# Kernel tuning notes

Hardware: AMD Instinct MI355X
Metric: run time of the kernel (lower is better)

The kernel has to match this reference:

```python
import jax, jax.numpy as jnp
import numpy as np

E = 8       # expert_number
TOP_K = 2


def setup_inputs() -> dict:
    key = jax.random.key(0)
    ks = jax.random.split(key, 5)
    B, S, D, H = 4, 2048, 1024, 4096
    scale = 0.02
    return {
        "x": jax.random.normal(ks[0], (B, S, D), dtype=jnp.float32),
        "gate_w": jax.random.normal(ks[1], (D, E), dtype=jnp.float32) * scale,
        "gate_b": jnp.zeros((E,), dtype=jnp.float32),
        "w1": jax.random.normal(ks[2], (E, D, H), dtype=jnp.float32) * scale,
        "b1": jnp.zeros((E, H), dtype=jnp.float32),
        "w2": jax.random.normal(ks[3], (E, H, D), dtype=jnp.float32) * scale,
        "b2": jnp.zeros((E, D), dtype=jnp.float32),
    }


def reference(x, gate_w, gate_b, w1, b1, w2, b2):
    B, S, D = x.shape
    h = x.reshape(-1, D)                                   # [T, D]

    # Router: softmax in fp32, top-k, renormalize (matches torch code)
    router_logits = h @ gate_w + gate_b                    # [T, E]
    probs = jax.nn.softmax(router_logits.astype(jnp.float32), axis=-1)
    rw, sel = jax.lax.top_k(probs, TOP_K)                  # [T, K] each
    rw = rw / rw.sum(axis=-1, keepdims=True)
    rw = rw.astype(h.dtype)

    # Per-token combine weight for each expert (0 if not selected): [T, E]
    we = (jax.nn.one_hot(sel, E, dtype=h.dtype) * rw[..., None]).sum(axis=1)

    out = jnp.zeros_like(h)
    for e in range(E):  # fixed small expert count; per-expert GEMM + weighted combine
        mid = jax.nn.gelu(h @ w1[e] + b1[e], approximate=False)  # [T, H]
        ye = mid @ w2[e] + b2[e]                                 # [T, D]
        out = out + we[:, e:e + 1] * ye

    return out.reshape(B, S, D), router_logits
```

## Files before the change

kernel.cpp:

```cpp
#include <hip/hip_runtime.h>
#include <hip/hip_bf16.h>
#include <math.h>

#define T_TOKENS 8192
#define DDIM 1024
#define HDIM 4096
#define NEXP 8
#define CAP 8192
#define MAXTILES 136

typedef __bf16 bf16;
typedef __bf16 bf16x4 __attribute__((ext_vector_type(4)));
typedef __bf16 bf16x8 __attribute__((ext_vector_type(8)));
typedef float  floatx16 __attribute__((ext_vector_type(16)));

__device__ static inline void async_load16(const void* g, void* l)
{
    __builtin_amdgcn_global_load_lds(
        (const __attribute__((address_space(1))) void*)g,
        (__attribute__((address_space(3))) void*)l, 16, 0, 0);
}

__global__ void router_kernel(const float* __restrict__ x,
                              const float* __restrict__ gw,
                              const float* __restrict__ gbias,
                              float* __restrict__ logits_out,
                              int* counts, int* token_of, float* wtab,
                              int* selpack)
{
    int t = blockIdx.x * 4 + (threadIdx.x >> 6);
    int l = threadIdx.x & 63;
    const float4* xr = (const float4*)(x + (size_t)t * DDIM);

    float p[NEXP];
#pragma unroll
    for (int e = 0; e < NEXP; ++e) p[e] = 0.f;

#pragma unroll
    for (int it = 0; it < 4; ++it) {
        int d4 = it * 64 + l;
        float4 v = xr[d4];
        float vv[4] = {v.x, v.y, v.z, v.w};
#pragma unroll
        for (int j = 0; j < 4; ++j) {
            const float4* g4 = (const float4*)(gw + (size_t)(d4 * 4 + j) * NEXP);
            float4 ga = g4[0], gb4 = g4[1];
            p[0] += vv[j] * ga.x;  p[1] += vv[j] * ga.y;
            p[2] += vv[j] * ga.z;  p[3] += vv[j] * ga.w;
            p[4] += vv[j] * gb4.x; p[5] += vv[j] * gb4.y;
            p[6] += vv[j] * gb4.z; p[7] += vv[j] * gb4.w;
        }
    }
#pragma unroll
    for (int e = 0; e < NEXP; ++e) {
#pragma unroll
        for (int off = 32; off; off >>= 1) p[e] += __shfl_xor(p[e], off);
        p[e] += gbias[e];
    }
    if (l < NEXP) logits_out[(size_t)t * NEXP + l] = p[l];

    if (l == 0) {
        int e0 = 0;
#pragma unroll
        for (int e = 1; e < NEXP; ++e) if (p[e] > p[e0]) e0 = e;
        int e1 = -1;
#pragma unroll
        for (int e = 0; e < NEXP; ++e) {
            if (e == e0) continue;
            if (e1 < 0 || p[e] > p[e1]) e1 = e;
        }
        float w0 = 1.f / (1.f + expf(p[e1] - p[e0]));
        float w1 = 1.f / (1.f + expf(p[e0] - p[e1]));
        int s0 = atomicAdd(&counts[e0], 1);
        int s1 = atomicAdd(&counts[e1], 1);
        token_of[e0 * CAP + s0] = t;
        token_of[e1 * CAP + s1] = t;
        wtab[e0 * CAP + s0] = w0;
        wtab[e1 * CAP + s1] = w1;
        selpack[t] = e0 | (e1 << 8);
    }
}

__global__ void offsets_kernel(const int* __restrict__ counts,
                               int* __restrict__ offsets,
                               int* __restrict__ tiles)
{
    if (threadIdx.x == 0) {
        int tmp[MAXTILES];
        int a = 0, nt = 0;
        for (int e = 0; e < NEXP; ++e) {
            offsets[e] = a;
            for (int r = 0; r < counts[e]; r += 128)
                tmp[nt++] = (e << 24) | (a + r);
            a += counts[e];
        }
        offsets[NEXP] = a;
        int per = (nt + 7) >> 3;
        for (int p = 0; p < MAXTILES; ++p) {
            int c = p & 7, k = p >> 3;
            int src = c * per + k;
            tiles[p] = (k < per && src < nt) ? tmp[src] : -1;
        }
    }
}

__global__ void gather_kernel(const float* __restrict__ x,
                              const int* __restrict__ offsets,
                              const int* __restrict__ token_of,
                              bf16* __restrict__ xg)
{
    int row = blockIdx.x * 4 + (threadIdx.x >> 6);
    int l = threadIdx.x & 63;
    int e = 0;
#pragma unroll
    for (int i = 1; i < NEXP; ++i) e += (row >= offsets[i]);
    int t = token_of[e * CAP + (row - offsets[e])];
    const float4* src = (const float4*)(x + (size_t)t * DDIM);
    bf16x4* dst = (bf16x4*)(xg + (size_t)row * DDIM);
#pragma unroll
    for (int it = 0; it < 4; ++it) {
        float4 v = src[it * 64 + l];
        bf16x4 b;
        b[0] = (bf16)v.x; b[1] = (bf16)v.y; b[2] = (bf16)v.z; b[3] = (bf16)v.w;
        dst[it * 64 + l] = b;
    }
}

__global__ void transpose_cvt_kernel(const float* __restrict__ in,
                                     bf16* __restrict__ out, int R, int C)
{
    __shared__ bf16 tile[64][68];
    int e = blockIdx.z;
    const float* src = in + (size_t)e * R * C;
    bf16* dst = out + (size_t)e * R * C;
    int r0 = blockIdx.y * 64, c0 = blockIdx.x * 64;
    int t = threadIdx.x;
    int lr = t >> 4, c4 = t & 15;
#pragma unroll
    for (int it = 0; it < 4; ++it) {
        int r = lr + it * 16;
        float4 v = *(const float4*)(src + (size_t)(r0 + r) * C + c0 + c4 * 4);
        bf16x4 b;
        b[0] = (bf16)v.x; b[1] = (bf16)v.y; b[2] = (bf16)v.z; b[3] = (bf16)v.w;
        *(bf16x4*)(&tile[r][c4 * 4]) = b;
    }
    __syncthreads();
    int oc = t >> 3, rseg = (t & 7) * 8;
#pragma unroll
    for (int it = 0; it < 2; ++it) {
        int c = oc + it * 32;
        bf16x8 v;
#pragma unroll
        for (int j = 0; j < 8; ++j) v[j] = tile[rseg + j][c];
        *(bf16x8*)(dst + (size_t)(c0 + c) * R + r0 + rseg) = v;
    }
}

template<int KTOT>
__device__ static inline void stage_tile(const bf16* __restrict__ gbase,
                                         bf16* lds, int wave, int lane, int valid)
{
#pragma unroll
    for (int it = 0; it < 4; ++it) {
        int rbase = wave * 32 + it * 8;
        int rloc  = rbase + (lane >> 3);
        int grow  = rloc < valid ? rloc : (valid - 1);
        int chunk = (lane & 7) ^ (rloc & 7);
        const bf16* g = gbase + (size_t)grow * KTOT + chunk * 8;
        async_load16(g, lds + rbase * 64);
    }
}

__device__ static inline float fast_gelu(float v)
{
    float z = v * (2.302236479f + 0.1029451170f * v * v);
    float ex = __builtin_amdgcn_exp2f(z);
    return v * ex * __builtin_amdgcn_rcpf(ex + 1.f);
}

#define GEMM_CORE(KTOT)                                                        \
    int tid = threadIdx.x;                                                     \
    int lane = tid & 63, wave = tid >> 6;                                      \
    int wr = wave >> 1, wc = wave & 1;                                         \
    int m32 = lane & 31, khalf = lane >> 5;                                    \
    int swz = m32 & 7;                                                         \
    floatx16 acc[2][2];                                                        \
    _Pragma("unroll") for (int i = 0; i < 2; ++i)                              \
    _Pragma("unroll") for (int j = 0; j < 2; ++j)                              \
    _Pragma("unroll") for (int r = 0; r < 16; ++r) acc[i][j][r] = 0.f;         \
    for (int k0 = 0; k0 < KTOT; k0 += 64) {                                    \
        stage_tile<KTOT>(A + k0, As, wave, lane, valid);                       \
        stage_tile<KTOT>(B + k0, Bs, wave, lane, 128);                         \
        __syncthreads();                                                       \
        _Pragma("unroll") for (int s = 0; s < 4; ++s) {                        \
            int pofs = (((2 * s + khalf) ^ swz) * 8);                          \
            bf16x8 af[2], bfr[2];                                              \
            _Pragma("unroll") for (int i = 0; i < 2; ++i)                      \
                af[i] = *(const bf16x8*)(&As[(wr * 64 + i * 32 + m32) * 64 + pofs]); \
            _Pragma("unroll") for (int j = 0; j < 2; ++j)                      \
                bfr[j] = *(const bf16x8*)(&Bs[(wc * 64 + j * 32 + m32) * 64 + pofs]); \
            _Pragma("unroll") for (int i = 0; i < 2; ++i)                      \
            _Pragma("unroll") for (int j = 0; j < 2; ++j)                      \
                acc[i][j] = __builtin_amdgcn_mfma_f32_32x32x16_bf16(           \
                    af[i], bfr[j], acc[i][j], 0, 0, 0);                        \
        }                                                                      \
        __syncthreads();                                                       \
    }

__global__ __launch_bounds__(256, 4)
void moe_gemm1(const bf16* __restrict__ Abase, const bf16* __restrict__ Bbase,
               const float* __restrict__ bias, bf16* __restrict__ Out,
               const int* __restrict__ tiles, const int* __restrict__ offsets)
{
    int info = tiles[blockIdx.x];
    if (info < 0) return;
    int e = info >> 24, row0 = info & 0xffffff;
    int valid = offsets[e + 1] - row0; if (valid > 128) valid = 128;
    int n0 = blockIdx.y * 128;

    const bf16* A = Abase + (size_t)row0 * DDIM;
    const bf16* B = Bbase + (size_t)e * HDIM * DDIM + (size_t)n0 * DDIM;
    const float* bvec = bias + (size_t)e * HDIM + n0;

    __shared__ __align__(16) bf16 As[128 * 64];
    __shared__ __align__(16) bf16 Bs[128 * 64];

    GEMM_CORE(DDIM)

#pragma unroll
    for (int i = 0; i < 2; ++i) {
#pragma unroll
        for (int j = 0; j < 2; ++j) {
            int lcol = wc * 64 + j * 32 + m32;
            float bj = bvec[lcol];
#pragma unroll
            for (int r = 0; r < 16; ++r) {
                int lrow = wr * 64 + i * 32 + (r & 3) + 8 * (r >> 2) + 4 * khalf;
                if (lrow >= valid) continue;
                float v = acc[i][j][r] + bj;
                Out[(size_t)(row0 + lrow) * HDIM + n0 + lcol] = (bf16)fast_gelu(v);
            }
        }
    }
}

__global__ __launch_bounds__(256, 4)
void moe_gemm2(const bf16* __restrict__ Abase, const bf16* __restrict__ Bbase,
               const float* __restrict__ bias, float* __restrict__ out,
               const int* __restrict__ tiles, const int* __restrict__ offsets,
               const int* __restrict__ token_of, const float* __restrict__ wtab)
{
    int info = tiles[blockIdx.x];
    if (info < 0) return;
    int e = info >> 24, row0 = info & 0xffffff;
    int valid = offsets[e + 1] - row0; if (valid > 128) valid = 128;
    int n0 = blockIdx.y * 128;

    const bf16* A = Abase + (size_t)row0 * HDIM;
    const bf16* B = Bbase + (size_t)e * DDIM * HDIM + (size_t)n0 * HDIM;
    const float* bvec = bias + (size_t)e * DDIM + n0;

    __shared__ __align__(16) bf16 As[128 * 64];
    __shared__ __align__(16) bf16 Bs[128 * 64];

    GEMM_CORE(HDIM)

    int*   tokS = (int*)As;
    float* wgtS = (float*)As + 128;
    if (tid < valid) {
        int s = row0 + tid - offsets[e];
        tokS[tid] = token_of[e * CAP + s];
        wgtS[tid] = wtab[e * CAP + s];
    }
    __syncthreads();

#pragma unroll
    for (int i = 0; i < 2; ++i) {
#pragma unroll
        for (int j = 0; j < 2; ++j) {
            int lcol = wc * 64 + j * 32 + m32;
            float bj = bvec[lcol];
#pragma unroll
            for (int r = 0; r < 16; ++r) {
                int lrow = wr * 64 + i * 32 + (r & 3) + 8 * (r >> 2) + 4 * khalf;
                if (lrow >= valid) continue;
                float v = acc[i][j][r] + bj;
                unsafeAtomicAdd(out + (size_t)tokS[lrow] * DDIM + n0 + lcol,
                                wgtS[lrow] * v);
            }
        }
    }
}

extern "C" void kernel_launch(void* const* d_in, const int* in_sizes, int n_in,
                              void* d_out, int out_size, void* d_ws, size_t ws_size,
                              hipStream_t stream)
{
    (void)in_sizes; (void)n_in; (void)out_size; (void)ws_size;
    const float* x  = (const float*)d_in[0];
    const float* gw = (const float*)d_in[1];
    const float* gb = (const float*)d_in[2];
    const float* w1 = (const float*)d_in[3];
    const float* b1 = (const float*)d_in[4];
    const float* w2 = (const float*)d_in[5];
    const float* b2 = (const float*)d_in[6];
    float* out    = (float*)d_out;
    float* logits = out + (size_t)T_TOKENS * DDIM;

    char* ws = (char*)d_ws;
    const size_t MB = 1024 * 1024;
    int*   counts   = (int*)(ws + 0);
    int*   offsets  = (int*)(ws + 256);
    int*   tiles    = (int*)(ws + 512);
    int*   selpack  = (int*)(ws + 4096);
    int*   token_of = (int*)(ws + 4096 + 64 * 1024);
    float* wtab     = (float*)(ws + 4096 + 320 * 1024);
    bf16*  xg  = (bf16*)(ws + 1 * MB);
    bf16*  w1b = (bf16*)(ws + 33 * MB);
    bf16*  w2b = (bf16*)(ws + 97 * MB);
    bf16*  mid = (bf16*)(ws + 161 * MB);

    hipMemsetAsync(counts, 0, 32, stream);
    hipMemsetAsync(out, 0, (size_t)T_TOKENS * DDIM * sizeof(float), stream);

    router_kernel<<<T_TOKENS / 4, 256, 0, stream>>>(x, gw, gb, logits, counts,
                                                    token_of, wtab, selpack);
    offsets_kernel<<<1, 64, 0, stream>>>(counts, offsets, tiles);
    gather_kernel<<<2 * T_TOKENS / 4, 256, 0, stream>>>(x, offsets, token_of, xg);
    transpose_cvt_kernel<<<dim3(HDIM / 64, DDIM / 64, NEXP), 256, 0, stream>>>(
        w1, w1b, DDIM, HDIM);
    transpose_cvt_kernel<<<dim3(DDIM / 64, HDIM / 64, NEXP), 256, 0, stream>>>(
        w2, w2b, HDIM, DDIM);
    moe_gemm1<<<dim3(MAXTILES, HDIM / 128), 256, 0, stream>>>(
        xg, w1b, b1, mid, tiles, offsets);
    moe_gemm2<<<dim3(MAXTILES, DDIM / 128), 256, 0, stream>>>(
        mid, w2b, b2, out, tiles, offsets, token_of, wtab);
}
```

Before: 1.049 ms.

## Switch GEMMs to 16x16x32 MFMA and merge router with weight transposes

Both expert GEMMs move from 32x32x16 to 16x16x32 bf16 MFMA, using a 4x4 grid of 16x16 accumulators per wave with new LDS fragment indexing and epilogue row mapping. The router and the two weight transpose/convert kernels are fused into one launch with block-index dispatch, removing two launches and letting router work overlap the transposes. The unused selpack write is dropped. The new MFMA shape changes LDS read patterns and instruction count, which may help or hurt the GEMM inner loop.

```diff
diff --git a/kernel.cpp b/kernel.cpp
--- a/kernel.cpp
+++ b/kernel.cpp
@@ -12,7 +12,7 @@
 typedef __bf16 bf16;
 typedef __bf16 bf16x4 __attribute__((ext_vector_type(4)));
 typedef __bf16 bf16x8 __attribute__((ext_vector_type(8)));
-typedef float  floatx16 __attribute__((ext_vector_type(16)));
+typedef float  floatx4 __attribute__((ext_vector_type(4)));
 
 __device__ static inline void async_load16(const void* g, void* l)
 {
@@ -21,63 +21,106 @@
         (__attribute__((address_space(3))) void*)l, 16, 0, 0);
 }
 
-__global__ void router_kernel(const float* __restrict__ x,
-                              const float* __restrict__ gw,
-                              const float* __restrict__ gbias,
-                              float* __restrict__ logits_out,
-                              int* counts, int* token_of, float* wtab,
-                              int* selpack)
-{
-    int t = blockIdx.x * 4 + (threadIdx.x >> 6);
-    int l = threadIdx.x & 63;
-    const float4* xr = (const float4*)(x + (size_t)t * DDIM);
-
-    float p[NEXP];
-#pragma unroll
-    for (int e = 0; e < NEXP; ++e) p[e] = 0.f;
-
+__global__ void prep_kernel(const float* __restrict__ w1,
+                            const float* __restrict__ w2,
+                            bf16* __restrict__ w1b,
+                            bf16* __restrict__ w2b,
+                            const float* __restrict__ x,
+                            const float* __restrict__ gw,
+                            const float* __restrict__ gbias,
+                            float* __restrict__ logits_out,
+                            int* counts, int* token_of, float* wtab)
+{
+    if (blockIdx.x >= 16384) {
+        int t = (blockIdx.x - 16384) * 4 + (threadIdx.x >> 6);
+        int l = threadIdx.x & 63;
+        const float4* xr = (const float4*)(x + (size_t)t * DDIM);
+
+        float p[NEXP];
+#pragma unroll
+        for (int e = 0; e < NEXP; ++e) p[e] = 0.f;
+#pragma unroll
+        for (int it = 0; it < 4; ++it) {
+            int d4 = it * 64 + l;
+            float4 v = xr[d4];
+            float vv[4] = {v.x, v.y, v.z, v.w};
+#pragma unroll
+            for (int j = 0; j < 4; ++j) {
+                const float4* g4 = (const float4*)(gw + (size_t)(d4 * 4 + j) * NEXP);
+                float4 ga = g4[0], gb4 = g4[1];
+                p[0] += vv[j] * ga.x;  p[1] += vv[j] * ga.y;
+                p[2] += vv[j] * ga.z;  p[3] += vv[j] * ga.w;
+                p[4] += vv[j] * gb4.x; p[5] += vv[j] * gb4.y;
+                p[6] += vv[j] * gb4.z; p[7] += vv[j] * gb4.w;
+            }
+        }
+#pragma unroll
+        for (int e = 0; e < NEXP; ++e) {
+#pragma unroll
+            for (int off = 32; off; off >>= 1) p[e] += __shfl_xor(p[e], off);
+            p[e] += gbias[e];
+        }
+        if (l < NEXP) logits_out[(size_t)t * NEXP + l] = p[l];
+
+        if (l == 0) {
+            int e0 = 0;
+#pragma unroll
+            for (int e = 1; e < NEXP; ++e) if (p[e] > p[e0]) e0 = e;
+            int e1 = -1;
+#pragma unroll
+            for (int e = 0; e < NEXP; ++e) {
+                if (e == e0) continue;
+                if (e1 < 0 || p[e] > p[e1]) e1 = e;
+            }
+            float w0 = 1.f / (1.f + expf(p[e1] - p[e0]));
+            float w1w = 1.f / (1.f + expf(p[e0] - p[e1]));
+            int s0 = atomicAdd(&counts[e0], 1);
+            int s1 = atomicAdd(&counts[e1], 1);
+            token_of[e0 * CAP + s0] = t;
+            token_of[e1 * CAP + s1] = t;
+            wtab[e0 * CAP + s0] = w0;
+            wtab[e1 * CAP + s1] = w1w;
+        }
+        return;
+    }
+
+    __shared__ bf16 tile[64][68];
+    int b = blockIdx.x;
+    int R, C, e, tr, tc;
+    const float* src;
+    bf16* dst;
+    if (b < 8192) {
+        R = DDIM; C = HDIM;
+        e = b >> 10; int tt = b & 1023;
+        tc = tt & 63; tr = tt >> 6;
+        src = w1 + (size_t)e * R * C; dst = w1b + (size_t)e * R * C;
+    } else {
+        b -= 8192;
+        R = HDIM; C = DDIM;
+        e = b >> 10; int tt = b & 1023;
+        tc = tt & 15; tr = tt >> 4;
+        src = w2 + (size_t)e * R * C; dst = w2b + (size_t)e * R * C;
+    }
+    int r0 = tr * 64, c0 = tc * 64;
+    int t = threadIdx.x;
+    int lr = t >> 4, c4 = t & 15;
 #pragma unroll
     for (int it = 0; it < 4; ++it) {
-        int d4 = it * 64 + l;
-        float4 v = xr[d4];
-        float vv[4] = {v.x, v.y, v.z, v.w};
-#pragma unroll
-        for (int j = 0; j < 4; ++j) {
-            const float4* g4 = (const float4*)(gw + (size_t)(d4 * 4 + j) * NEXP);
-            float4 ga = g4[0], gb4 = g4[1];
-            p[0] += vv[j] * ga.x;  p[1] += vv[j] * ga.y;
-            p[2] += vv[j] * ga.z;  p[3] += vv[j] * ga.w;
-            p[4] += vv[j] * gb4.x; p[5] += vv[j] * gb4.y;
-            p[6] += vv[j] * gb4.z; p[7] += vv[j] * gb4.w;
-        }
-    }
-#pragma unroll
-    for (int e = 0; e < NEXP; ++e) {
-#pragma unroll
-        for (int off = 32; off; off >>= 1) p[e] += __shfl_xor(p[e], off);
-        p[e] += gbias[e];
-    }
-    if (l < NEXP) logits_out[(size_t)t * NEXP + l] = p[l];
-
-    if (l == 0) {
-        int e0 = 0;
-#pragma unroll
-        for (int e = 1; e < NEXP; ++e) if (p[e] > p[e0]) e0 = e;
-        int e1 = -1;
-#pragma unroll
-        for (int e = 0; e < NEXP; ++e) {
-            if (e == e0) continue;
-            if (e1 < 0 || p[e] > p[e1]) e1 = e;
-        }
-        float w0 = 1.f / (1.f + expf(p[e1] - p[e0]));
-        float w1 = 1.f / (1.f + expf(p[e0] - p[e1]));
-        int s0 = atomicAdd(&counts[e0], 1);
-        int s1 = atomicAdd(&counts[e1], 1);
-        token_of[e0 * CAP + s0] = t;
-        token_of[e1 * CAP + s1] = t;
-        wtab[e0 * CAP + s0] = w0;
-        wtab[e1 * CAP + s1] = w1;
-        selpack[t] = e0 | (e1 << 8);
+        int r = lr + it * 16;
+        float4 v = *(const float4*)(src + (size_t)(r0 + r) * C + c0 + c4 * 4);
+        bf16x4 bb;
+        bb[0] = (bf16)v.x; bb[1] = (bf16)v.y; bb[2] = (bf16)v.z; bb[3] = (bf16)v.w;
+        *(bf16x4*)(&tile[r][c4 * 4]) = bb;
+    }
+    __syncthreads();
+    int oc = t >> 3, rseg = (t & 7) * 8;
+#pragma unroll
+    for (int it = 0; it < 2; ++it) {
+        int c = oc + it * 32;
+        bf16x8 v;
+#pragma unroll
+        for (int j = 0; j < 8; ++j) v[j] = tile[rseg + j][c];
+        *(bf16x8*)(dst + (size_t)(c0 + c) * R + r0 + rseg) = v;
     }
 }
 
@@ -126,36 +169,6 @@
     }
 }
 
-__global__ void transpose_cvt_kernel(const float* __restrict__ in,
-                                     bf16* __restrict__ out, int R, int C)
-{
-    __shared__ bf16 tile[64][68];
-    int e = blockIdx.z;
-    const float* src = in + (size_t)e * R * C;
-    bf16* dst = out + (size_t)e * R * C;
-    int r0 = blockIdx.y * 64, c0 = blockIdx.x * 64;
-    int t = threadIdx.x;
-    int lr = t >> 4, c4 = t & 15;
-#pragma unroll
-    for (int it = 0; it < 4; ++it) {
-        int r = lr + it * 16;
-        float4 v = *(const float4*)(src + (size_t)(r0 + r) * C + c0 + c4 * 4);
-        bf16x4 b;
-        b[0] = (bf16)v.x; b[1] = (bf16)v.y; b[2] = (bf16)v.z; b[3] = (bf16)v.w;
-        *(bf16x4*)(&tile[r][c4 * 4]) = b;
-    }
-    __syncthreads();
-    int oc = t >> 3, rseg = (t & 7) * 8;
-#pragma unroll
-    for (int it = 0; it < 2; ++it) {
-        int c = oc + it * 32;
-        bf16x8 v;
-#pragma unroll
-        for (int j = 0; j < 8; ++j) v[j] = tile[rseg + j][c];
-        *(bf16x8*)(dst + (size_t)(c0 + c) * R + r0 + rseg) = v;
-    }
-}
-
 template<int KTOT>
 __device__ static inline void stage_tile(const bf16* __restrict__ gbase,
                                          bf16* lds, int wave, int lane, int valid)
@@ -182,26 +195,27 @@
     int tid = threadIdx.x;                                                     \
     int lane = tid & 63, wave = tid >> 6;                                      \
     int wr = wave >> 1, wc = wave & 1;                                         \
-    int m32 = lane & 31, khalf = lane >> 5;                                    \
-    int swz = m32 & 7;                                                         \
-    floatx16 acc[2][2];                                                        \
-    _Pragma("unroll") for (int i = 0; i < 2; ++i)                              \
-    _Pragma("unroll") for (int j = 0; j < 2; ++j)                              \
-    _Pragma("unroll") for (int r = 0; r < 16; ++r) acc[i][j][r] = 0.f;         \
+    int m16 = lane & 15, quad = lane >> 4;                                     \
+    int swz = m16 & 7;                                                         \
+    floatx4 acc[4][4];                                                         \
+    _Pragma("unroll") for (int i = 0; i < 4; ++i)                              \
+    _Pragma("unroll") for (int j = 0; j < 4; ++j)                              \
+    _Pragma("unroll") for (int r = 0; r < 4; ++r) acc[i][j][r] = 0.f;          \
     for (int k0 = 0; k0 < KTOT; k0 += 64) {                                    \
         stage_tile<KTOT>(A + k0, As, wave, lane, valid);                       \
         stage_tile<KTOT>(B + k0, Bs, wave, lane, 128);                         \
         __syncthreads();                                                       \
-        _Pragma("unroll") for (int s = 0; s < 4; ++s) {                        \
-            int pofs = (((2 * s + khalf) ^ swz) * 8);                          \
-            bf16x8 af[2], bfr[2];                                              \
-            _Pragma("unroll") for (int i = 0; i < 2; ++i)                      \
-                af[i] = *(const bf16x8*)(&As[(wr * 64 + i * 32 + m32) * 64 + pofs]); \
-            _Pragma("unroll") for (int j = 0; j < 2; ++j)                      \
-                bfr[j] = *(const bf16x8*)(&Bs[(wc * 64 + j * 32 + m32) * 64 + pofs]); \
-            _Pragma("unroll") for (int i = 0; i < 2; ++i)                      \
-            _Pragma("unroll") for (int j = 0; j < 2; ++j)                      \
-                acc[i][j] = __builtin_amdgcn_mfma_f32_32x32x16_bf16(           \
+        _Pragma("unroll") for (int ks = 0; ks < 64; ks += 32) {                \
+            int cbase = (ks >> 3) + quad;                                      \
+            int pchunk = (cbase ^ swz) * 8;                                    \
+            bf16x8 af[4], bfr[4];                                              \
+            _Pragma("unroll") for (int i = 0; i < 4; ++i)                      \
+                af[i] = *(const bf16x8*)(&As[(wr * 64 + i * 16 + m16) * 64 + pchunk]); \
+            _Pragma("unroll") for (int j = 0; j < 4; ++j)                      \
+                bfr[j] = *(const bf16x8*)(&Bs[(wc * 64 + j * 16 + m16) * 64 + pchunk]); \
+            _Pragma("unroll") for (int i = 0; i < 4; ++i)                      \
+            _Pragma("unroll") for (int j = 0; j < 4; ++j)                      \
+                acc[i][j] = __builtin_amdgcn_mfma_f32_16x16x32_bf16(           \
                     af[i], bfr[j], acc[i][j], 0, 0, 0);                        \
         }                                                                      \
         __syncthreads();                                                       \
@@ -228,17 +242,16 @@
     GEMM_CORE(DDIM)
 
 #pragma unroll
-    for (int i = 0; i < 2; ++i) {
-#pragma unroll
-        for (int j = 0; j < 2; ++j) {
-            int lcol = wc * 64 + j * 32 + m32;
-            float bj = bvec[lcol];
-#pragma unroll
-            for (int r = 0; r < 16; ++r) {
-                int lrow = wr * 64 + i * 32 + (r & 3) + 8 * (r >> 2) + 4 * khalf;
-                if (lrow >= valid) continue;
-                float v = acc[i][j][r] + bj;
-                Out[(size_t)(row0 + lrow) * HDIM + n0 + lcol] = (bf16)fast_gelu(v);
+    for (int i = 0; i < 4; ++i) {
+#pragma unroll
+        for (int r = 0; r < 4; ++r) {
+            int lrow = wr * 64 + i * 16 + quad * 4 + r;
+            if (lrow >= valid) continue;
+            size_t orow = (size_t)(row0 + lrow) * HDIM + n0;
+#pragma unroll
+            for (int j = 0; j < 4; ++j) {
+                int lcol = wc * 64 + j * 16 + m16;
+                Out[orow + lcol] = (bf16)fast_gelu(acc[i][j][r] + bvec[lcol]);
             }
         }
     }
@@ -275,18 +288,17 @@
     __syncthreads();
 
 #pragma unroll
-    for (int i = 0; i < 2; ++i) {
-#pragma unroll
-        for (int j = 0; j < 2; ++j) {
-            int lcol = wc * 64 + j * 32 + m32;
-            float bj = bvec[lcol];
-#pragma unroll
-            for (int r = 0; r < 16; ++r) {
-                int lrow = wr * 64 + i * 32 + (r & 3) + 8 * (r >> 2) + 4 * khalf;
-                if (lrow >= valid) continue;
-                float v = acc[i][j][r] + bj;
-                unsafeAtomicAdd(out + (size_t)tokS[lrow] * DDIM + n0 + lcol,
-                                wgtS[lrow] * v);
+    for (int i = 0; i < 4; ++i) {
+#pragma unroll
+        for (int r = 0; r < 4; ++r) {
+            int lrow = wr * 64 + i * 16 + quad * 4 + r;
+            if (lrow >= valid) continue;
+            float* orow = out + (size_t)tokS[lrow] * DDIM + n0;
+            float wgt = wgtS[lrow];
+#pragma unroll
+            for (int j = 0; j < 4; ++j) {
+                int lcol = wc * 64 + j * 16 + m16;
+                unsafeAtomicAdd(orow + lcol, wgt * (acc[i][j][r] + bvec[lcol]));
             }
         }
     }
@@ -312,7 +324,6 @@
     int*   counts   = (int*)(ws + 0);
     int*   offsets  = (int*)(ws + 256);
     int*   tiles    = (int*)(ws + 512);
-    int*   selpack  = (int*)(ws + 4096);
     int*   token_of = (int*)(ws + 4096 + 64 * 1024);
     float* wtab     = (float*)(ws + 4096 + 320 * 1024);
     bf16*  xg  = (bf16*)(ws + 1 * MB);
@@ -323,14 +334,10 @@
     hipMemsetAsync(counts, 0, 32, stream);
     hipMemsetAsync(out, 0, (size_t)T_TOKENS * DDIM * sizeof(float), stream);
 
-    router_kernel<<<T_TOKENS / 4, 256, 0, stream>>>(x, gw, gb, logits, counts,
-                                                    token_of, wtab, selpack);
+    prep_kernel<<<16384 + T_TOKENS / 4, 256, 0, stream>>>(
+        w1, w2, w1b, w2b, x, gw, gb, logits, counts, token_of, wtab);
     offsets_kernel<<<1, 64, 0, stream>>>(counts, offsets, tiles);
     gather_kernel<<<2 * T_TOKENS / 4, 256, 0, stream>>>(x, offsets, token_of, xg);
-    transpose_cvt_kernel<<<dim3(HDIM / 64, DDIM / 64, NEXP), 256, 0, stream>>>(
-        w1, w1b, DDIM, HDIM);
-    transpose_cvt_kernel<<<dim3(DDIM / 64, HDIM / 64, NEXP), 256, 0, stream>>>(
-        w2, w2b, HDIM, DDIM);
     moe_gemm1<<<dim3(MAXTILES, HDIM / 128), 256, 0, stream>>>(
         xg, w1b, b1, mid, tiles, offsets);
     moe_gemm2<<<dim3(MAXTILES, DDIM / 128), 256, 0, stream>>>(
```

Result: faster. 986.5 us (-5.9%).
